# Optimization experiments

Hardware: AMD Instinct MI355X
Metric: run time of the kernel (lower is better)

The kernel has to match this reference:

```python
import jax, jax.numpy as jnp
import numpy as np

N = 57254   # num nodes == embedding vocab (hardcoded in module)
E = 916064  # num edges = N * avg_degree(16)
D = 128     # node_input_dim == node_hidden_dim
H = 8       # num_heads
O = D // H  # out_feats per head = 16
B, T = 64, 512


def setup_inputs() -> dict:
    key = jax.random.key(0)
    ks = jax.random.split(key, 13)
    f = lambda k, s: jax.random.normal(k, s, jnp.float32) * 0.05
    return {
        "emb": f(ks[0], (N, D)),
        "W0": f(ks[1], (D, H * O)), "al0": f(ks[2], (H, O)), "ar0": f(ks[3], (H, O)), "b0": f(ks[4], (H * O,)),
        "W1": f(ks[5], (D, H * O)), "al1": f(ks[6], (H, O)), "ar1": f(ks[7], (H, O)), "b1": f(ks[8], (H * O,)),
        "n_feat": jax.random.randint(ks[9], (N,), 0, N),
        "src": jax.random.randint(ks[10], (E,), 0, N),
        "dst": jax.random.randint(ks[11], (E,), 0, N),
        "x": jax.random.randint(ks[12], (B, T), 0, N),
    }


def _gat_layer(h, W, al, ar, b, src, dst, activate):
    # h: (N, D) -> z: (N, H, O)
    z = (h @ W).reshape(N, H, O)
    el = jnp.sum(z * al, axis=-1)            # (N, H)
    er = jnp.sum(z * ar, axis=-1)            # (N, H)
    e = jax.nn.leaky_relu(el[src] + er[dst], 0.2)  # (E, H) edge scores
    # segment softmax over incoming edges per destination node
    m = jax.ops.segment_max(e, dst, num_segments=N)   # (N, H)
    a = jnp.exp(e - m[dst])
    s = jax.ops.segment_sum(a, dst, num_segments=N)   # (N, H)
    alpha = a / s[dst]                                # (E, H)
    rst = jax.ops.segment_sum(alpha[:, :, None] * z[src], dst, num_segments=N)  # (N, H, O)
    # residual (identity since in_feats == H*O) + bias
    rst = rst + h.reshape(N, H, O) + b.reshape(1, H, O)
    if activate:
        rst = jax.nn.leaky_relu(rst, 0.01)  # F.leaky_relu default slope
    return rst.reshape(N, H * O)


def reference(emb, W0, al0, ar0, b0, W1, al1, ar1, b1, n_feat, src, dst, x):
    h = emb[n_feat]                                        # (N, D) embedding lookup
    h = _gat_layer(h, W0, al0, ar0, b0, src, dst, True)    # layer 0 (activation)
    h = _gat_layer(h, W1, al1, ar1, b1, src, dst, False)   # layer 1 (no activation)
    # F.normalize(p=2, eps=1e-5)
    nrm = jnp.sqrt(jnp.sum(h * h, axis=-1, keepdims=True))
    v = h / jnp.maximum(nrm, 1e-5)
    # broadcast-expand + flat index == direct gather of node embeddings
    return v[x]                                            # (B, T, D)
```

## Files before the change

kernel.cpp:

```cpp
#include <hip/hip_runtime.h>

#define N_NODES 57254
#define N_EDGES 916064
#define DIM 128
#define NHEAD 8
#define BT (64*512)
#define NBKT 224
#define NCHUNK 256
#define CHUNK 3579

typedef __attribute__((ext_vector_type(8))) short short8v;
typedef __attribute__((ext_vector_type(4))) float f32x4;
typedef __attribute__((ext_vector_type(2))) float f32x2;

#if defined(__has_builtin)
#  if __has_builtin(__builtin_amdgcn_cvt_pk_f32_fp8) && __has_builtin(__builtin_amdgcn_cvt_pk_fp8_f32)
#    define USE_FP8 1
#  endif
#endif
#ifndef USE_FP8
#  define USE_FP8 0
#endif

#define ZSCALE 16.0f
#define ZSCALE_INV (1.0f/16.0f)

static __device__ __forceinline__ unsigned short f2bf(float f){
  unsigned int b = __builtin_bit_cast(unsigned int, f);
  b += 0x7fffu + ((b >> 16) & 1u);
  return (unsigned short)(b >> 16);
}
static __device__ __forceinline__ float bf2f(unsigned short u){
  unsigned int b = ((unsigned int)u) << 16;
  return __builtin_bit_cast(float, b);
}
static __device__ __forceinline__ float lo16f(unsigned int zz){
  return __builtin_bit_cast(float, zz << 16);
}
static __device__ __forceinline__ float hi16f(unsigned int zz){
  return __builtin_bit_cast(float, zz & 0xffff0000u);
}

#if USE_FP8
#define ZB 1
static __device__ __forceinline__ void z_store(unsigned char* Zp, float v){
  unsigned u = (unsigned)__builtin_amdgcn_cvt_pk_fp8_f32(v*ZSCALE, v*ZSCALE, 0, false);
  *Zp = (unsigned char)(u & 0xffu);
}
static __device__ __forceinline__ f32x2 z_pair(unsigned short w){
  return __builtin_amdgcn_cvt_pk_f32_fp8((int)(unsigned)w, false);
}
#else
#define ZB 2
static __device__ __forceinline__ void z_store(unsigned char* Zp, float v){
  *(unsigned short*)Zp = f2bf(v);
}
static __device__ __forceinline__ f32x2 z_pair(unsigned zz){
  f32x2 r; r.x = lo16f(zz)*ZSCALE; r.y = hi16f(zz)*ZSCALE; return r;
}
#endif


__global__ __launch_bounds__(256) void p1hist(const int* __restrict__ dst,
                                              int* __restrict__ bh){
  __shared__ int h[NBKT];
  int t = threadIdx.x, c = blockIdx.x;
  if (t < NBKT) h[t] = 0;
  __syncthreads();
  int lo = c*CHUNK, hi = lo + CHUNK; if (hi > N_EDGES) hi = N_EDGES;
  for (int i = lo + t; i < hi; i += 256)
    atomicAdd(&h[((unsigned)dst[i]) >> 8], 1);
  __syncthreads();
  if (t < NBKT) bh[t*NCHUNK + c] = h[t];
}

__global__ void scan_partial(const int* __restrict__ in, int* __restrict__ out,
                             int* __restrict__ bsum, int n){
  __shared__ int sm[256];
  int tid = threadIdx.x;
  int i = blockIdx.x*256 + tid;
  int v = (i < n) ? in[i] : 0;
  sm[tid] = v;
  __syncthreads();
  #pragma unroll
  for (int d = 1; d < 256; d <<= 1){
    int add = (tid >= d) ? sm[tid - d] : 0;
    __syncthreads();
    sm[tid] += add;
    __syncthreads();
  }
  if (i < n) out[i] = sm[tid] - v;
  if (tid == 255) bsum[blockIdx.x] = sm[255];
}

__global__ void scan_add2(int* __restrict__ out, const int* __restrict__ bsum,
                          int nb, int n){
  __shared__ int sm[256];
  int t = threadIdx.x, b = blockIdx.x;
  sm[t] = (t < b && t < nb) ? bsum[t] : 0;
  __syncthreads();
  #pragma unroll
  for (int d = 128; d; d >>= 1){
    if (t < d) sm[t] += sm[t + d];
    __syncthreads();
  }
  int i = b*256 + t;
  if (i < n) out[i] += sm[0];
}

__global__ __launch_bounds__(256) void p1scat(const int* __restrict__ src,
                                              const int* __restrict__ dst,
                                              const int* __restrict__ bases,
                                              unsigned* __restrict__ ebuf){
  __shared__ unsigned stage[CHUNK];
  __shared__ short bkt_of[CHUNK];
  __shared__ int lh[256], smm[256], ls[NBKT+1], cur[NBKT], gb[NBKT];
  int t = threadIdx.x, c = blockIdx.x;
  lh[t] = 0;
  __syncthreads();
  int lo = c*CHUNK, hi = lo + CHUNK; if (hi > N_EDGES) hi = N_EDGES;
  int len = hi - lo;
  for (int i = lo + t; i < hi; i += 256)
    atomicAdd(&lh[((unsigned)dst[i]) >> 8], 1);
  __syncthreads();
  int v = lh[t];
  smm[t] = v;
  __syncthreads();
  #pragma unroll
  for (int d = 1; d < 256; d <<= 1){
    int add = (t >= d) ? smm[t - d] : 0;
    __syncthreads();
    smm[t] += add;
    __syncthreads();
  }
  if (t < NBKT){ ls[t] = smm[t] - v; cur[t] = smm[t] - v; gb[t] = bases[t*NCHUNK + c]; }
  if (t == 255) ls[NBKT] = smm[255];
  __syncthreads();
  if (t < NBKT){
    int e0 = ls[t], e1 = ls[t+1];
    for (int k = e0; k < e1; ++k) bkt_of[k] = (short)t;
  }
  __syncthreads();
  for (int i = lo + t; i < hi; i += 256){
    unsigned d = (unsigned)dst[i];
    int b = d >> 8;
    int pos = atomicAdd(&cur[b], 1);
    stage[pos] = (((unsigned)src[i]) << 16) | (d & 255u);
  }
  __syncthreads();
  for (int k = t; k < len; k += 256){
    int b = bkt_of[k];
    ebuf[gb[b] + (k - ls[b])] = stage[k];
  }
}

__global__ __launch_bounds__(256) void p2fine(const unsigned* __restrict__ ebuf,
                                              const int* __restrict__ bases,
                                              int* __restrict__ offs,
                                              int* __restrict__ csr){
  __shared__ int cnt[256], sm[256], loff[256], cur[256];
  int t = threadIdx.x, b = blockIdx.x;
  int bstart = bases[b*NCHUNK];
  int bend   = (b < NBKT-1) ? bases[(b+1)*NCHUNK] : N_EDGES;
  cnt[t] = 0;
  __syncthreads();
  for (int i = bstart + t; i < bend; i += 256)
    atomicAdd(&cnt[ebuf[i] & 255u], 1);
  __syncthreads();
  int v = cnt[t];
  sm[t] = v;
  __syncthreads();
  #pragma unroll
  for (int d = 1; d < 256; d <<= 1){
    int add = (t >= d) ? sm[t - d] : 0;
    __syncthreads();
    sm[t] += add;
    __syncthreads();
  }
  loff[t] = sm[t] - v;
  cur[t]  = bstart + sm[t] - v;
  int nlo = b*256;
  int nn  = N_NODES - nlo; if (nn > 256) nn = 256;
  if (t < nn) offs[nlo + t] = bstart + loff[t];
  if (b == NBKT-1 && t == 0) offs[N_NODES] = N_EDGES;
  __syncthreads();
  for (int i = bstart + t; i < bend; i += 256){
    unsigned e = ebuf[i];
    int pos = atomicAdd(&cur[e & 255u], 1);
    csr[pos] = (int)(e >> 16);
  }
}

__global__ void twt_kernel(const float* __restrict__ W0, const float* __restrict__ W1,
                           unsigned short* __restrict__ Wt0, unsigned short* __restrict__ Wt1){
  int t = blockIdx.x*256 + threadIdx.x;
  int which = t >> 14;
  int i = t & 16383;
  int c = i >> 7, k = i & 127;
  const float* W = which ? W1 : W0;
  unsigned short* Wt = which ? Wt1 : Wt0;
  Wt[i] = f2bf(W[k*128 + c]);
}

template<int MODE>
__global__ __launch_bounds__(256) void gemm_nt(
    const void* __restrict__ Av, const int* __restrict__ gidx,
    const unsigned short* __restrict__ Wt,
    unsigned char* __restrict__ Z,
    unsigned short* __restrict__ Hb)
{
  __shared__ unsigned short As[128*128];
  __shared__ unsigned short Bs[128*128];
  int t = threadIdx.x;
  int brow = blockIdx.x * 128;
  {
    int r = t >> 1, half = t & 1;
    int grow = brow + r;
    bool valid = grow < N_NODES;
    unsigned srcr = 0u;
    if (MODE == 0) srcr = valid ? (unsigned)gidx[grow] : 0u;
    #pragma unroll
    for (int j = 0; j < 8; ++j){
      int c = half*64 + j*8;
      short8v pk;
      if (MODE == 0){
        const float* arow = (const float*)Av + (size_t)srcr * DIM;
        float4 a0, a1;
        if (valid){ a0 = *(const float4*)(arow + c); a1 = *(const float4*)(arow + c + 4); }
        else { a0 = make_float4(0.f,0.f,0.f,0.f); a1 = a0; }
        pk[0]=(short)f2bf(a0.x); pk[1]=(short)f2bf(a0.y); pk[2]=(short)f2bf(a0.z); pk[3]=(short)f2bf(a0.w);
        pk[4]=(short)f2bf(a1.x); pk[5]=(short)f2bf(a1.y); pk[6]=(short)f2bf(a1.z); pk[7]=(short)f2bf(a1.w);
        if (valid) *(short8v*)(Hb + (unsigned)grow*128u + c) = pk;
      } else {
        const unsigned short* A = (const unsigned short*)Av;
        if (valid) pk = *(const short8v*)(A + (unsigned)grow*128u + c);
        else       pk = (short8v){0,0,0,0,0,0,0,0};
      }
      int byte = (r*256 + c*2) ^ ((r & 7) << 4);
      *(short8v*)((char*)As + byte) = pk;
    }
    int cc = t >> 1, khalf = t & 1;
    #pragma unroll
    for (int j = 0; j < 8; ++j){
      int k0 = khalf*64 + j*8;
      short8v w = *(const short8v*)(Wt + cc*128 + k0);
      int byte = (cc*256 + k0*2) ^ ((cc & 7) << 4);
      *(short8v*)((char*)Bs + byte) = w;
    }
  }
  __syncthreads();
  int w = t >> 6, lane = t & 63;
  f32x4 acc[2][8];
  #pragma unroll
  for (int m=0;m<2;m++)
    #pragma unroll
    for (int n=0;n<8;n++) acc[m][n] = (f32x4){0.f,0.f,0.f,0.f};
  #pragma unroll
  for (int kk = 0; kk < 4; ++kk){
    int ks = kk*32 + (lane>>4)*8;
    short8v a[2], b[8];
    #pragma unroll
    for (int m=0;m<2;m++){
      int row = w*32 + m*16 + (lane & 15);
      int byte = (row*256 + ks*2) ^ ((row & 7) << 4);
      a[m] = *(const short8v*)((const char*)As + byte);
    }
    #pragma unroll
    for (int n=0;n<8;n++){
      int col = n*16 + (lane & 15);
      int byte = (col*256 + ks*2) ^ ((col & 7) << 4);
      b[n] = *(const short8v*)((const char*)Bs + byte);
    }
    #pragma unroll
    for (int m=0;m<2;m++)
      #pragma unroll
      for (int n=0;n<8;n++)
        acc[m][n] = __builtin_amdgcn_mfma_f32_16x16x32_bf16(a[m], b[n], acc[m][n], 0, 0, 0);
  }
  #pragma unroll
  for (int m=0;m<2;m++){
    int row_base = brow + w*32 + m*16 + ((lane>>4)<<2);
    #pragma unroll
    for (int r=0;r<4;r++){
      int grow = row_base + r;
      if (grow < N_NODES){
        #pragma unroll
        for (int n=0;n<8;n++)
          z_store(Z + ((unsigned)grow*128u + n*16 + (lane&15))*ZB, acc[m][n][r]);
      }
    }
  }
}

__global__ void eler_kernel(const unsigned char* __restrict__ Z,
                            const float* __restrict__ al, const float* __restrict__ ar,
                            unsigned short* __restrict__ el, float* __restrict__ er)
{
  int t = blockIdx.x*256 + threadIdx.x;
  if (t >= N_NODES*NHEAD) return;
  int h = t & 7;
  const unsigned char* zp = Z + ((unsigned)(t>>3)*128u + h*16)*ZB;
  float zv[16];
#if USE_FP8
  uint4 zw = *(const uint4*)zp;
  f32x2 p;
  p = z_pair((unsigned short)(zw.x & 0xffffu));      zv[0]=p.x;  zv[1]=p.y;
  p = __builtin_amdgcn_cvt_pk_f32_fp8((int)zw.x, true);  zv[2]=p.x;  zv[3]=p.y;
  p = z_pair((unsigned short)(zw.y & 0xffffu));      zv[4]=p.x;  zv[5]=p.y;
  p = __builtin_amdgcn_cvt_pk_f32_fp8((int)zw.y, true);  zv[6]=p.x;  zv[7]=p.y;
  p = z_pair((unsigned short)(zw.z & 0xffffu));      zv[8]=p.x;  zv[9]=p.y;
  p = __builtin_amdgcn_cvt_pk_f32_fp8((int)zw.z, true);  zv[10]=p.x; zv[11]=p.y;
  p = z_pair((unsigned short)(zw.w & 0xffffu));      zv[12]=p.x; zv[13]=p.y;
  p = __builtin_amdgcn_cvt_pk_f32_fp8((int)zw.w, true);  zv[14]=p.x; zv[15]=p.y;
#else
  short8v z0 = *(const short8v*)(zp);
  short8v z1 = *(const short8v*)(zp + 16);
  #pragma unroll
  for (int o = 0; o < 8; ++o){ zv[o] = bf2f((unsigned short)z0[o])*ZSCALE; zv[8+o] = bf2f((unsigned short)z1[o])*ZSCALE; }
#endif
  float sl = 0.f, sr = 0.f;
  #pragma unroll
  for (int o = 0; o < 16; ++o){
    sl += zv[o] * al[h*16+o]; sr += zv[o] * ar[h*16+o];
  }
  el[t] = f2bf(sl*ZSCALE_INV); er[t] = sr*ZSCALE_INV;
}

__global__ __launch_bounds__(256) void edge_agg(
    const unsigned char* __restrict__ Z, const unsigned short* __restrict__ el,
    const float* __restrict__ er, const int* __restrict__ off,
    const int* __restrict__ csr, const unsigned short* __restrict__ Hin,
    const float* __restrict__ bias, unsigned short* __restrict__ Hout,
    int activate)
{
  int tid  = threadIdx.x;
  int lane = tid & 63;
  int n    = __builtin_amdgcn_readfirstlane((int)(blockIdx.x*4 + (tid >> 6)));
  if (n >= N_NODES) return;
  int head = lane >> 3;

  int lo = off[n], hi = off[n+1];
  float ern = er[(unsigned)n*8u + head];
  float acc0a=0.f, acc0b=0.f, acc1a=0.f, acc1b=0.f, sacca=0.f, saccb=0.f;
  const unsigned lidx = (unsigned)(lane*2);

  for (int base = lo; base < hi; base += 16){
    int s[16]; float x[16]; unsigned short zz[16]; float wv[16];
    #pragma unroll
    for (int j=0;j<16;++j){
      int idx = base + j;
      s[j] = csr[idx < hi ? idx : hi-1];
    }
    #pragma unroll
    for (int j=0;j<16;++j) x[j] = bf2f(el[(unsigned)s[j]*8u + head]) + ern;
    #pragma unroll
    for (int j=0;j<16;++j) zz[j] = *(const unsigned short*)(Z + ((unsigned)s[j]*128u + lidx)*ZB);
    #pragma unroll
    for (int j=0;j<16;++j){
      float xv = fmaxf(x[j], 0.2f*x[j]);
      wv[j] = (base + j < hi) ? __expf(xv) : 0.f;
    }
    #pragma unroll
    for (int j=0;j<16;j+=2){
      f32x2 z0 = z_pair(zz[j]);
      f32x2 z1 = z_pair(zz[j+1]);
      sacca += wv[j];        saccb += wv[j+1];
      acc0a += wv[j]*z0.x;   acc0b += wv[j+1]*z1.x;
      acc1a += wv[j]*z0.y;   acc1b += wv[j+1]*z1.y;
    }
  }
  float sacc = sacca + saccb;
  float acc0 = acc0a + acc0b;
  float acc1 = acc1a + acc1b;
  float inv = (hi > lo) ? (ZSCALE_INV / sacc) : 0.f;
  unsigned hv = *(const unsigned*)(Hin + (unsigned)n*128u + lidx);
  int d = lane*2;
  float r0 = acc0*inv + lo16f(hv) + bias[d];
  float r1 = acc1*inv + hi16f(hv) + bias[d+1];
  if (activate){
    r0 = (r0 > 0.f) ? r0 : 0.01f*r0;
    r1 = (r1 > 0.f) ? r1 : 0.01f*r1;
  }
  unsigned outv = ((unsigned)f2bf(r1) << 16) | (unsigned)f2bf(r0);
  *(unsigned*)(Hout + (unsigned)n*128u + lidx) = outv;
}

__global__ __launch_bounds__(256) void norm_gather(const unsigned short* __restrict__ H,
    const int* __restrict__ x, float* __restrict__ out)
{
  int row = blockIdx.x*4 + (threadIdx.x >> 6);
  if (row >= BT) return;
  int lane = threadIdx.x & 63;
  unsigned xi = (unsigned)x[row];
  unsigned hv = *(const unsigned*)(H + xi*128u + (unsigned)(lane*2));
  float v0 = lo16f(hv), v1 = hi16f(hv);
  float ss = v0*v0 + v1*v1;
  #pragma unroll
  for (int m = 32; m; m >>= 1) ss += __shfl_xor(ss, m, 64);
  float sc = 1.f / fmaxf(sqrtf(ss), 1e-5f);
  int d = lane*2;
  out[(size_t)row*128 + d]     = v0*sc;
  out[(size_t)row*128 + d + 1] = v1*sc;
}

extern "C" void kernel_launch(void* const* d_in, const int* in_sizes, int n_in,
                              void* d_out, int out_size, void* d_ws, size_t ws_size,
                              hipStream_t stream)
{
  const float* emb = (const float*)d_in[0];
  const float* W0  = (const float*)d_in[1];
  const float* al0 = (const float*)d_in[2];
  const float* ar0 = (const float*)d_in[3];
  const float* b0  = (const float*)d_in[4];
  const float* W1  = (const float*)d_in[5];
  const float* al1 = (const float*)d_in[6];
  const float* ar1 = (const float*)d_in[7];
  const float* b1  = (const float*)d_in[8];
  const int* n_feat = (const int*)d_in[9];
  const int* srcv = (const int*)d_in[10];
  const int* dstv = (const int*)d_in[11];
  const int* xv   = (const int*)d_in[12];
  float* out = (float*)d_out;

  char* p = (char*)d_ws;
  auto alloc = [&](size_t b)->char*{ char* q = p; p += (b + 255) & ~(size_t)255; return q; };
  unsigned char*  Z   = (unsigned char*)alloc((size_t)N_NODES*128*ZB);
  unsigned short* H1b = (unsigned short*)alloc((size_t)N_NODES*128*2);
  unsigned short* Hb0 = (unsigned short*)alloc((size_t)N_NODES*128*2);
  int* offs  = (int*)alloc((size_t)(N_NODES+1)*4);
  int* csr   = (int*)alloc((size_t)N_EDGES*4);
  unsigned* ebuf = (unsigned*)alloc((size_t)N_EDGES*4);
  int* bh    = (int*)alloc((size_t)NBKT*NCHUNK*4);
  int* bsum  = (int*)alloc(256*4);
  unsigned short* Wt0 = (unsigned short*)alloc(128*128*2);
  unsigned short* Wt1 = (unsigned short*)alloc(128*128*2);
  unsigned short* el = (unsigned short*)ebuf;
  float* er = (float*)(((char*)ebuf) + (((size_t)N_NODES*8*2 + 255) & ~(size_t)255));

  const int NSCAN = NBKT*NCHUNK;

  p1hist<<<NCHUNK, 256, 0, stream>>>(dstv, bh);
  scan_partial<<<NSCAN/256, 256, 0, stream>>>(bh, bh, bsum, NSCAN);
  scan_add2<<<NSCAN/256, 256, 0, stream>>>(bh, bsum, NSCAN/256, NSCAN);
  p1scat<<<NCHUNK, 256, 0, stream>>>(srcv, dstv, bh, ebuf);
  p2fine<<<NBKT, 256, 0, stream>>>(ebuf, bh, offs, csr);

  twt_kernel<<<128, 256, 0, stream>>>(W0, W1, Wt0, Wt1);

  int gemm_grid = (N_NODES + 127)/128;
  int agg_grid  = (N_NODES + 3)/4;
  int eler_grid = (N_NODES*8 + 255)/256;

  gemm_nt<0><<<gemm_grid, 256, 0, stream>>>(emb, n_feat, Wt0, Z, Hb0);
  eler_kernel<<<eler_grid, 256, 0, stream>>>(Z, al0, ar0, el, er);
  edge_agg<<<agg_grid, 256, 0, stream>>>(Z, el, er, offs, csr, Hb0, b0, H1b, 1);
  gemm_nt<1><<<gemm_grid, 256, 0, stream>>>(H1b, nullptr, Wt1, Z, nullptr);
  eler_kernel<<<eler_grid, 256, 0, stream>>>(Z, al1, ar1, el, er);
  edge_agg<<<agg_grid, 256, 0, stream>>>(Z, el, er, offs, csr, H1b, b1, H1b, 0);
  norm_gather<<<(BT + 3)/4, 256, 0, stream>>>(H1b, xv, out);
}
```

Baseline: 171.3 us.

## Pad CSR rows to multiples of 8 and share edge weights via swizzle

CSR construction now pads each destination row up to a multiple of 8 entries, filling the padding with a dummy node index. That dummy node gets el = -inf so its weight is zero. In edge_agg, each lane computes one edge's exp weight (exp2 with log2e folded into el/er) and broadcasts it to the rest of its head group with ds_swizzle. This replaces every lane recomputing 16 weights, cutting redundant el gathers and exp work and removing the bounds checks. The cost is extra padded CSR traffic, an extra dummy Z row, and swizzle latency. There is also a risk that the dummy Z row is never written.

```diff
diff --git a/kernel.cpp b/kernel.cpp
--- a/kernel.cpp
+++ b/kernel.cpp
@@ -8,6 +8,7 @@
 #define NBKT 224
 #define NCHUNK 256
 #define CHUNK 3579
+#define LOG2E 1.4426950408889634f
 
 typedef __attribute__((ext_vector_type(8))) short short8v;
 typedef __attribute__((ext_vector_type(4))) float f32x4;
@@ -157,18 +158,21 @@
 __global__ __launch_bounds__(256) void p2fine(const unsigned* __restrict__ ebuf,
                                               const int* __restrict__ bases,
                                               int* __restrict__ offs,
+                                              int* __restrict__ pcnt,
                                               int* __restrict__ csr){
-  __shared__ int cnt[256], sm[256], loff[256], cur[256];
+  __shared__ int cnt[256], sm[256], plo[256], cur[256];
   int t = threadIdx.x, b = blockIdx.x;
   int bstart = bases[b*NCHUNK];
   int bend   = (b < NBKT-1) ? bases[(b+1)*NCHUNK] : N_EDGES;
+  int pbstart = bstart + b*1792;
   cnt[t] = 0;
   __syncthreads();
   for (int i = bstart + t; i < bend; i += 256)
     atomicAdd(&cnt[ebuf[i] & 255u], 1);
   __syncthreads();
   int v = cnt[t];
-  sm[t] = v;
+  int pv = (v + 7) & ~7;
+  sm[t] = pv;
   __syncthreads();
   #pragma unroll
   for (int d = 1; d < 256; d <<= 1){
@@ -177,17 +181,21 @@
     sm[t] += add;
     __syncthreads();
   }
-  loff[t] = sm[t] - v;
-  cur[t]  = bstart + sm[t] - v;
+  plo[t] = sm[t] - pv;
+  cur[t] = pbstart + plo[t];
   int nlo = b*256;
   int nn  = N_NODES - nlo; if (nn > 256) nn = 256;
-  if (t < nn) offs[nlo + t] = bstart + loff[t];
-  if (b == NBKT-1 && t == 0) offs[N_NODES] = N_EDGES;
+  if (t < nn){ offs[nlo + t] = pbstart + plo[t]; pcnt[nlo + t] = pv; }
   __syncthreads();
   for (int i = bstart + t; i < bend; i += 256){
     unsigned e = ebuf[i];
     int pos = atomicAdd(&cur[e & 255u], 1);
     csr[pos] = (int)(e >> 16);
+  }
+  __syncthreads();
+  if (t < nn){
+    int end = pbstart + plo[t] + pv;
+    for (int k = cur[t]; k < end; ++k) csr[k] = N_NODES;
   }
 }
 
@@ -297,7 +305,10 @@
                             unsigned short* __restrict__ el, float* __restrict__ er)
 {
   int t = blockIdx.x*256 + threadIdx.x;
-  if (t >= N_NODES*NHEAD) return;
+  if (t >= N_NODES*NHEAD){
+    if (t < (N_NODES+1)*NHEAD){ el[t] = 0xFF80u; er[t] = 0.f; }
+    return;
+  }
   int h = t & 7;
   const unsigned char* zp = Z + ((unsigned)(t>>3)*128u + h*16)*ZB;
   float zv[16];
@@ -323,56 +334,56 @@
   for (int o = 0; o < 16; ++o){
     sl += zv[o] * al[h*16+o]; sr += zv[o] * ar[h*16+o];
   }
-  el[t] = f2bf(sl*ZSCALE_INV); er[t] = sr*ZSCALE_INV;
+  el[t] = f2bf(sl*(ZSCALE_INV*LOG2E)); er[t] = sr*(ZSCALE_INV*LOG2E);
 }
 
 __global__ __launch_bounds__(256) void edge_agg(
     const unsigned char* __restrict__ Z, const unsigned short* __restrict__ el,
-    const float* __restrict__ er, const int* __restrict__ off,
-    const int* __restrict__ csr, const unsigned short* __restrict__ Hin,
-    const float* __restrict__ bias, unsigned short* __restrict__ Hout,
-    int activate)
+    const float* __restrict__ er, const int* __restrict__ offs,
+    const int* __restrict__ pcnt, const int* __restrict__ csr,
+    const unsigned short* __restrict__ Hin, const float* __restrict__ bias,
+    unsigned short* __restrict__ Hout, int activate)
 {
   int tid  = threadIdx.x;
   int lane = tid & 63;
   int n    = __builtin_amdgcn_readfirstlane((int)(blockIdx.x*4 + (tid >> 6)));
   if (n >= N_NODES) return;
-  int head = lane >> 3;
-
-  int lo = off[n], hi = off[n+1];
+  int head  = lane >> 3;
+  int eslot = lane & 7;
+
+  int lo = offs[n], pc = pcnt[n];
   float ern = er[(unsigned)n*8u + head];
-  float acc0a=0.f, acc0b=0.f, acc1a=0.f, acc1b=0.f, sacca=0.f, saccb=0.f;
+  float acc0 = 0.f, acc1 = 0.f, sacc_p = 0.f;
   const unsigned lidx = (unsigned)(lane*2);
 
-  for (int base = lo; base < hi; base += 16){
-    int s[16]; float x[16]; unsigned short zz[16]; float wv[16];
-    #pragma unroll
-    for (int j=0;j<16;++j){
-      int idx = base + j;
-      s[j] = csr[idx < hi ? idx : hi-1];
-    }
-    #pragma unroll
-    for (int j=0;j<16;++j) x[j] = bf2f(el[(unsigned)s[j]*8u + head]) + ern;
-    #pragma unroll
-    for (int j=0;j<16;++j) zz[j] = *(const unsigned short*)(Z + ((unsigned)s[j]*128u + lidx)*ZB);
-    #pragma unroll
-    for (int j=0;j<16;++j){
-      float xv = fmaxf(x[j], 0.2f*x[j]);
-      wv[j] = (base + j < hi) ? __expf(xv) : 0.f;
-    }
-    #pragma unroll
-    for (int j=0;j<16;j+=2){
-      f32x2 z0 = z_pair(zz[j]);
-      f32x2 z1 = z_pair(zz[j+1]);
-      sacca += wv[j];        saccb += wv[j+1];
-      acc0a += wv[j]*z0.x;   acc0b += wv[j+1]*z1.x;
-      acc1a += wv[j]*z0.y;   acc1b += wv[j+1]*z1.y;
-    }
-  }
-  float sacc = sacca + saccb;
-  float acc0 = acc0a + acc0b;
-  float acc1 = acc1a + acc1b;
-  float inv = (hi > lo) ? (ZSCALE_INV / sacc) : 0.f;
+  for (int base = lo; base < lo + pc; base += 8){
+    unsigned sv = (unsigned)csr[base + eslot];
+    unsigned short zz[8];
+    #pragma unroll
+    for (int e = 0; e < 8; ++e){
+      int se = csr[base + e];
+      zz[e] = *(const unsigned short*)(Z + ((unsigned)se*128u + lidx)*ZB);
+    }
+    float x = bf2f(el[sv*8u + head]) + ern;
+    x = fmaxf(x, 0.2f*x);
+    float w = exp2f(x);
+    sacc_p += w;
+    int wi = __builtin_bit_cast(int, w);
+#define SWZ_STEP(E) { \
+      float we = __builtin_bit_cast(float, \
+          __builtin_amdgcn_ds_swizzle(wi, 0x18 | ((E)<<5))); \
+      f32x2 z = z_pair(zz[E]); \
+      acc0 += we*z.x; \
+      acc1 += we*z.y; }
+    SWZ_STEP(0) SWZ_STEP(1) SWZ_STEP(2) SWZ_STEP(3)
+    SWZ_STEP(4) SWZ_STEP(5) SWZ_STEP(6) SWZ_STEP(7)
+#undef SWZ_STEP
+  }
+  float sacc = sacc_p;
+  sacc += __shfl_xor(sacc, 1, 64);
+  sacc += __shfl_xor(sacc, 2, 64);
+  sacc += __shfl_xor(sacc, 4, 64);
+  float inv = (pc > 0) ? (ZSCALE_INV / sacc) : 0.f;
   unsigned hv = *(const unsigned*)(Hin + (unsigned)n*128u + lidx);
   int d = lane*2;
   float r0 = acc0*inv + lo16f(hv) + bias[d];
@@ -422,20 +433,23 @@
   const int* xv   = (const int*)d_in[12];
   float* out = (float*)d_out;
 
+  const int CSR_PAD = N_EDGES + NBKT*1792;
+
   char* p = (char*)d_ws;
   auto alloc = [&](size_t b)->char*{ char* q = p; p += (b + 255) & ~(size_t)255; return q; };
-  unsigned char*  Z   = (unsigned char*)alloc((size_t)N_NODES*128*ZB);
+  unsigned char*  Z   = (unsigned char*)alloc((size_t)(N_NODES+1)*128*ZB);
   unsigned short* H1b = (unsigned short*)alloc((size_t)N_NODES*128*2);
   unsigned short* Hb0 = (unsigned short*)alloc((size_t)N_NODES*128*2);
-  int* offs  = (int*)alloc((size_t)(N_NODES+1)*4);
-  int* csr   = (int*)alloc((size_t)N_EDGES*4);
+  int* offs  = (int*)alloc((size_t)N_NODES*4);
+  int* pcnt  = (int*)alloc((size_t)N_NODES*4);
+  int* csr   = (int*)alloc((size_t)CSR_PAD*4);
   unsigned* ebuf = (unsigned*)alloc((size_t)N_EDGES*4);
   int* bh    = (int*)alloc((size_t)NBKT*NCHUNK*4);
   int* bsum  = (int*)alloc(256*4);
   unsigned short* Wt0 = (unsigned short*)alloc(128*128*2);
   unsigned short* Wt1 = (unsigned short*)alloc(128*128*2);
   unsigned short* el = (unsigned short*)ebuf;
-  float* er = (float*)(((char*)ebuf) + (((size_t)N_NODES*8*2 + 255) & ~(size_t)255));
+  float* er = (float*)(((char*)ebuf) + (((size_t)(N_NODES+1)*8*2 + 255) & ~(size_t)255));
 
   const int NSCAN = NBKT*NCHUNK;
 
@@ -443,19 +457,19 @@
   scan_partial<<<NSCAN/256, 256, 0, stream>>>(bh, bh, bsum, NSCAN);
   scan_add2<<<NSCAN/256, 256, 0, stream>>>(bh, bsum, NSCAN/256, NSCAN);
   p1scat<<<NCHUNK, 256, 0, stream>>>(srcv, dstv, bh, ebuf);
-  p2fine<<<NBKT, 256, 0, stream>>>(ebuf, bh, offs, csr);
+  p2fine<<<NBKT, 256, 0, stream>>>(ebuf, bh, offs, pcnt, csr);
 
   twt_kernel<<<128, 256, 0, stream>>>(W0, W1, Wt0, Wt1);
 
   int gemm_grid = (N_NODES + 127)/128;
   int agg_grid  = (N_NODES + 3)/4;
-  int eler_grid = (N_NODES*8 + 255)/256;
+  int eler_grid = ((N_NODES+1)*8 + 255)/256;
 
   gemm_nt<0><<<gemm_grid, 256, 0, stream>>>(emb, n_feat, Wt0, Z, Hb0);
   eler_kernel<<<eler_grid, 256, 0, stream>>>(Z, al0, ar0, el, er);
-  edge_agg<<<agg_grid, 256, 0, stream>>>(Z, el, er, offs, csr, Hb0, b0, H1b, 1);
+  edge_agg<<<agg_grid, 256, 0, stream>>>(Z, el, er, offs, pcnt, csr, Hb0, b0, H1b, 1);
   gemm_nt<1><<<gemm_grid, 256, 0, stream>>>(H1b, nullptr, Wt1, Z, nullptr);
   eler_kernel<<<eler_grid, 256, 0, stream>>>(Z, al1, ar1, el, er);
-  edge_agg<<<agg_grid, 256, 0, stream>>>(Z, el, er, offs, csr, H1b, b1, H1b, 0);
+  edge_agg<<<agg_grid, 256, 0, stream>>>(Z, el, er, offs, pcnt, csr, H1b, b1, H1b, 0);
   norm_gather<<<(BT + 3)/4, 256, 0, stream>>>(H1b, xv, out);
 }
```

Measured after the change: 160.3 us (median of 2 runs). 6.4% less time.
